# Kernel tuning notes

Measured on AMD Instinct MI355X. Metric: run time of the kernel, lower is better.

The kernel has to match this reference:

```python
import jax, jax.numpy as jnp
import numpy as np

EPS = 1e-5

def inorm(x, w, b):
    # InstanceNorm1d over token dim (axis=1), per (batch, feature); biased var
    m = x.mean(axis=1, keepdims=True)
    v = ((x - m) ** 2).mean(axis=1, keepdims=True)
    return (x - m) / jnp.sqrt(v + EPS) * w + b

def setup_inputs() -> dict:
    B, N, D, FH = 2, 512, 128, 512
    key = jax.random.key(0)
    ks = iter(jax.random.split(key, 48))
    rn = lambda shape, s=0.05: jax.random.normal(next(ks), shape, jnp.float32) * s
    inp = {
        'row_emb': jax.random.normal(next(ks), (B, N, D), jnp.float32),
        'col_emb': jax.random.normal(next(ks), (B, N, D), jnp.float32),
        'cost_mat': jax.random.uniform(next(ks), (B, N, N), jnp.float32),
        'coords': jax.random.uniform(next(ks), (B, N, 2), jnp.float32),
        'alpha': jnp.ones((1,), jnp.float32),
        # instance norm affine params (weight~1, bias~0)
        'n1_w': 1.0 + rn((D,)), 'n1_b': rn((D,)),
        'n2_w': 1.0 + rn((D,)), 'n2_b': rn((D,)),
        'n3_w': 1.0 + rn((D,)), 'n3_b': rn((D,)),
        'fn1_w': 1.0 + rn((D,)), 'fn1_b': rn((D,)),
        'fn2_w': 1.0 + rn((D,)), 'fn2_b': rn((D,)),
        # AFTFull projections (stored (in,out))
        'q_w': rn((D, D)), 'q_b': rn((D,)),
        'k_w': rn((D, D)), 'k_b': rn((D,)),
        'v_w': rn((D, D)), 'v_b': rn((D,)),
        'p_w': rn((D, D)), 'p_b': rn((D,)),
        'mhc_w': rn((D, D)), 'mhc_b': rn((D,)),
        # DistAngleFusion MLPs
        'dist_w1': rn((1, D)), 'dist_b1': rn((D,)),
        'dist_w2': rn((D, D)), 'dist_b2': rn((D,)),
        'ang_w1': rn((1, D)), 'ang_b1': rn((D,)),
        'ang_w2': rn((D, D)), 'ang_b2': rn((D,)),
        'gate_w': rn((2 * D, 1)), 'gate_b': rn((1,)),
        'outlin_w': rn((D, 1)), 'outlin_b': rn((1,)),
        # FeedForward
        'ffn_w1': rn((D, FH)), 'ffn_b1': rn((FH,)),
        'ffn_w2': rn((FH, D)), 'ffn_b2': rn((D,)),
    }
    return inp

def reference(row_emb, col_emb, cost_mat, coords, alpha,
              n1_w, n1_b, n2_w, n2_b, n3_w, n3_b, fn1_w, fn1_b, fn2_w, fn2_b,
              q_w, q_b, k_w, k_b, v_w, v_b, p_w, p_b, mhc_w, mhc_b,
              dist_w1, dist_b1, dist_w2, dist_b2,
              ang_w1, ang_b1, ang_w2, ang_b2,
              gate_w, gate_b, outlin_w, outlin_b,
              ffn_w1, ffn_b1, ffn_w2, ffn_b2):
    rn = inorm(row_emb, n1_w, n1_b)
    cn = inorm(col_emb, n2_w, n2_b)

    # DistAngleFusion: adapt_bias (B,N,N)
    diff = coords[:, :, None, :] - coords[:, None, :, :]  # (B,N,N,2)
    angles = jnp.arctan2(diff[..., 1], diff[..., 0])
    dist_e = jax.nn.relu(cost_mat[..., None] @ dist_w1 + dist_b1) @ dist_w2 + dist_b2  # (B,N,N,D)
    angle_e = jax.nn.relu(angles[..., None] @ ang_w1 + ang_b1) @ ang_w2 + ang_b2
    g = jax.nn.sigmoid(jnp.concatenate([dist_e, angle_e], axis=-1) @ gate_w + gate_b)  # (B,N,N,1)
    fused = g * dist_e + (1.0 - g) * angle_e
    adapt_bias = (fused @ outlin_w + outlin_b)[..., 0] * alpha  # (B,N,N)

    # AFTFull
    Q = jax.nn.sigmoid(rn @ q_w + q_b)          # (B,N,H)
    K = jax.nn.softmax(cn @ k_w + k_b, axis=1)  # softmax over tokens
    V = cn @ v_w + v_b
    eab = jnp.exp(jax.nn.softmax(adapt_bias, axis=-1))  # (B,N,N)
    eK = jnp.exp(K)
    num = jnp.einsum('bnm,bmh->bnh', eab, eK * V)
    den = jnp.einsum('bnm,bmh->bnh', eab, eK)
    Yt = (Q * (num / den)) @ p_w + p_b

    mh = inorm(Yt @ mhc_w + mhc_b, n3_w, n3_b)

    # TransformerFFN with instance norms
    x = inorm(rn + mh, fn1_w, fn1_b)
    ff = jax.nn.relu(x @ ffn_w1 + ffn_b1) @ ffn_w2 + ffn_b2
    return inorm(x + ff, fn2_w, fn2_b)
```

## Files before the change

### kernel.cpp

```cpp
#include <hip/hip_runtime.h>
#include <hip/hip_bf16.h>
#include <math.h>

#define Bn  2
#define Nn  512
#define Dn  128
#define FHn 512
#define BND (Bn*Nn*Dn)

typedef __hip_bfloat16 bf16;

__device__ __forceinline__ float cvt(float x) { return x; }
__device__ __forceinline__ float cvt(bf16 x) { return __bfloat162float(x); }
__device__ __forceinline__ float sigmoidf_(float x) { return 1.0f / (1.0f + expf(-x)); }
__device__ __forceinline__ bool is_bf16(const void* alpha) {
    return ((const unsigned short*)alpha)[0] == 0x3F80;
}

#define S_ 131072
#define WS_Q    (0 * S_)
#define WS_K    (1 * S_)
#define WS_V    (2 * S_)
#define WS_EK   (3 * S_)
#define WS_EKV  (4 * S_)
#define WS_EAB  (5 * S_)
#define WS_MH   (1 * S_)
#define WS_T    (2 * S_)
#define WS_OP   (3 * S_)
#define WS_ST   (9 * S_)

#define ST_IN_SC   0
#define ST_IN_SH   512
#define ST_X_SC    2048
#define ST_X_SH    2304
#define ST_PRE     3072
#define P_SC       1024
#define ST_TAB     4224

#define TAB_ANG 644
#define TAB_N   1288

#define SMEM_FLOATS 2568

struct KP {
    const void *row, *col, *cost, *coords, *alpha;
    const void *n1w, *n1b, *n2w, *n2b, *n3w, *n3b, *f1w, *f1b, *f2w, *f2b;
    const void *qw, *qb, *kw, *kb, *vw, *vb, *pw, *pb, *mw, *mb;
    const void *dw1, *db1, *dw2, *db2, *aw1, *ab1, *aw2, *ab2, *gw, *gb, *ow, *ob;
    const void *ffw1, *ffb1, *ffw2, *ffb2;
    void* out;
    float* ws;
};

__device__ __forceinline__ void blk_sum2(float& s, float& ss, volatile float* scr) {
#pragma unroll
    for (int off = 32; off > 0; off >>= 1) { s += __shfl_down(s, off); ss += __shfl_down(ss, off); }
    __syncthreads();
    int wave = threadIdx.x >> 6, lane = threadIdx.x & 63;
    if (lane == 0) { scr[wave] = s; scr[4 + wave] = ss; }
    __syncthreads();
    s = scr[0] + scr[1] + scr[2] + scr[3];
    ss = scr[4] + scr[5] + scr[6] + scr[7];
}

__device__ __forceinline__ float blk_sum1(float v, volatile float* scr) {
#pragma unroll
    for (int off = 32; off > 0; off >>= 1) v += __shfl_down(v, off);
    __syncthreads();
    int wave = threadIdx.x >> 6, lane = threadIdx.x & 63;
    if (lane == 0) scr[wave] = v;
    __syncthreads();
    return scr[0] + scr[1] + scr[2] + scr[3];
}

__device__ __forceinline__ float blk_max1(float v, volatile float* scr) {
#pragma unroll
    for (int off = 32; off > 0; off >>= 1) v = fmaxf(v, __shfl_down(v, off));
    __syncthreads();
    int wave = threadIdx.x >> 6, lane = threadIdx.x & 63;
    if (lane == 0) scr[wave] = v;
    __syncthreads();
    return fmaxf(fmaxf(scr[0], scr[1]), fmaxf(scr[2], scr[3]));
}

template <typename T>
__device__ void build_tables(const T* w1p, const T* b1p, const T* w2p,
                             const T* owp, const T* gwp, float* gtab, float* smem) {
    int tid = threadIdx.x;
    float* W  = smem;
    float* Bb = smem + 128;
    float* U  = smem + 256;
    float* Vv = smem + 384;
    float* Tt = smem + 512;
    int* RK   = (int*)(smem + 640);
    if (tid < 128) {
        float u = 0.f, v = 0.f;
#pragma unroll 4
        for (int d = 0; d < Dn; ++d) {
            float w2 = cvt(w2p[tid * Dn + d]);
            u += w2 * cvt(owp[d]);
            v += w2 * cvt(gwp[d]);
        }
        float w = cvt(w1p[tid]), b = cvt(b1p[tid]);
        U[tid] = u; Vv[tid] = v; W[tid] = w; Bb[tid] = b;
        Tt[tid] = (w != 0.f) ? (-b / w) : 3.0e38f;
    }
    __syncthreads();
    if (tid < 128) {
        float tk = Tt[tid]; int r = 0;
        for (int j = 0; j < 128; ++j) {
            float tj = Tt[j];
            r += (tj < tk) || (tj == tk && j < tid);
        }
        RK[tid] = r;
        gtab[r] = tk;
    }
    __syncthreads();
    if (tid <= 128) {
        int si = tid;
        float slS = 0, inS = 0, slT = 0, inT = 0;
        for (int k = 0; k < 128; ++k) {
            float w = W[k];
            if (w == 0.f) {
                float rb = fmaxf(Bb[k], 0.f);
                inS += rb * U[k];
                inT += rb * Vv[k];
            } else {
                bool act = (w > 0.f) ? (RK[k] < si) : (RK[k] >= si);
                if (act) {
                    slS += w * U[k];  inS += Bb[k] * U[k];
                    slT += w * Vv[k]; inT += Bb[k] * Vv[k];
                }
            }
        }
        gtab[128 + si] = slS;
        gtab[257 + si] = inS;
        gtab[386 + si] = slT;
        gtab[515 + si] = inT;
    }
}

__device__ __forceinline__ int bsearch128(const float* T, float c) {
    int lo = 0, hi = 128;
    while (lo < hi) { int mid = (lo + hi) >> 1; if (T[mid] <= c) lo = mid + 1; else hi = mid; }
    return lo;
}

template <typename T>
__device__ void phase0(const KP& p, float* st, float* smem) {
    float* scr = smem + 2560;
    int cid = blockIdx.x;
    int tid = threadIdx.x;
    {
        int which = cid >> 8, b = (cid >> 7) & 1, d = cid & 127;
        const T* src = (const T*)(which ? p.col : p.row) + (size_t)b * Nn * Dn + d;
        float x0 = cvt(src[(size_t)tid * Dn]);
        float x1 = cvt(src[(size_t)(tid + 256) * Dn]);
        float s = x0 + x1, ss = x0 * x0 + x1 * x1;
        blk_sum2(s, ss, scr);
        if (tid == 0) {
            float m = s * (1.f / Nn);
            float v = fmaxf(ss * (1.f / Nn) - m * m, 0.f);
            float rstd = rsqrtf(v + 1e-5f);
            const T* w = which ? (const T*)p.n2w : (const T*)p.n1w;
            const T* bb = which ? (const T*)p.n2b : (const T*)p.n1b;
            float sc = rstd * cvt(w[d]);
            st[ST_IN_SC + cid] = sc;
            st[ST_IN_SH + cid] = cvt(bb[d]) - m * sc;
        }
    }
    __syncthreads();
    if (cid == 128) {
        const T* db2 = (const T*)p.db2; const T* ab2 = (const T*)p.ab2;
        const T* ow = (const T*)p.ow;   const T* gw = (const T*)p.gw;
        float d2 = 0.f, a2 = 0.f, o = 0.f, g0 = 0.f, g1 = 0.f;
        if (tid < 128) {
            d2 = cvt(db2[tid]); a2 = cvt(ab2[tid]);
            o = cvt(ow[tid]); g0 = cvt(gw[tid]); g1 = cvt(gw[Dn + tid]);
        }
        float cds = d2 * o, cdt = d2 * g0, cas = a2 * o, cat = a2 * g1;
        blk_sum2(cds, cdt, scr);
        blk_sum2(cas, cat, scr);
        if (tid == 0) {
            float* pre = st + ST_PRE;
            pre[P_SC + 0] = cds; pre[P_SC + 1] = cdt;
            pre[P_SC + 2] = cas; pre[P_SC + 3] = cat;
            pre[P_SC + 4] = cvt(((const T*)p.gb)[0]);
            pre[P_SC + 5] = cvt(((const T*)p.ob)[0]);
            pre[P_SC + 6] = cvt(((const T*)p.alpha)[0]);
        }
    } else if (cid == 129) {
        build_tables<T>((const T*)p.dw1, (const T*)p.db1, (const T*)p.dw2,
                        (const T*)p.ow, (const T*)p.gw, st + ST_TAB, smem);
    } else if (cid == 130) {
        build_tables<T>((const T*)p.aw1, (const T*)p.ab1, (const T*)p.aw2,
                        (const T*)p.ow, (const T*)p.gw + Dn, st + ST_TAB + TAB_ANG, smem);
    }
}

template <typename T>
__device__ void phase1(const KP& p, float* st, float* smem) {
    int tid = threadIdx.x;
    int r0 = blockIdx.x * 2;
    int b = r0 >> 9;
    const T* row = (const T*)p.row; const T* col = (const T*)p.col;
    float* ws = p.ws;
    float* Q = ws + WS_Q; float* Kraw = ws + WS_K; float* V = ws + WS_V;

    float* lr = smem;
    float* lc = smem + 256;
    float* redq = smem + 512;
    float* redk = smem + 1024;
    float* redv = smem + 1536;
    {
        int r = tid >> 7, d = tid & 127;
        float scR = st[ST_IN_SC + b * 128 + d],       shR = st[ST_IN_SH + b * 128 + d];
        float scC = st[ST_IN_SC + 256 + b * 128 + d], shC = st[ST_IN_SH + 256 + b * 128 + d];
        lr[r * 128 + d] = cvt(row[(size_t)(r0 + r) * Dn + d]) * scR + shR;
        lc[r * 128 + d] = cvt(col[(size_t)(r0 + r) * Dn + d]) * scC + shC;
    }
    __syncthreads();
    {
        int h = tid & 127, half = tid >> 7;
        const T* qw = (const T*)p.qw; const T* kw = (const T*)p.kw; const T* vw = (const T*)p.vw;
        float q0 = 0, q1 = 0, ka = 0, kb_ = 0, v0 = 0, v1 = 0;
        int ks = half * 64;
#pragma unroll 8
        for (int k = ks; k < ks + 64; ++k) {
            float wq = cvt(qw[k * Dn + h]);
            float wk = cvt(kw[k * Dn + h]);
            float wv = cvt(vw[k * Dn + h]);
            q0 += lr[k] * wq;        q1 += lr[128 + k] * wq;
            ka += lc[k] * wk;        kb_ += lc[128 + k] * wk;
            v0 += lc[k] * wv;        v1 += lc[128 + k] * wv;
        }
        redq[half * 256 + h] = q0;  redq[half * 256 + 128 + h] = q1;
        redk[half * 256 + h] = ka;  redk[half * 256 + 128 + h] = kb_;
        redv[half * 256 + h] = v0;  redv[half * 256 + 128 + h] = v1;
    }
    __syncthreads();
    if (tid < 128) {
        int h = tid;
        float bq = cvt(((const T*)p.qb)[h]);
        float bk = cvt(((const T*)p.kb)[h]);
        float bv = cvt(((const T*)p.vb)[h]);
#pragma unroll
        for (int r = 0; r < 2; ++r) {
            Q[(r0 + r) * Dn + h]    = sigmoidf_(redq[r * 128 + h] + redq[256 + r * 128 + h] + bq);
            Kraw[(r0 + r) * Dn + h] = redk[r * 128 + h] + redk[256 + r * 128 + h] + bk;
            V[(r0 + r) * Dn + h]    = redv[r * 128 + h] + redv[256 + r * 128 + h] + bv;
        }
    }
    __syncthreads();

    float* abv = smem;
    float* red = smem + 512;
    float* tab = smem + 768;
    const float* gtab = st + ST_TAB;
    for (int e = tid; e < TAB_N; e += 256) tab[e] = gtab[e];
    __syncthreads();
    float* eab = ws + WS_EAB;
    const float* pre = st + ST_PRE;
    float cds = pre[P_SC + 0], cdt = pre[P_SC + 1], cas = pre[P_SC + 2], cat = pre[P_SC + 3];
    float gbias = pre[P_SC + 4], obias = pre[P_SC + 5], alpha = pre[P_SC + 6];
    const T* cost = (const T*)p.cost;
    const T* coords = (const T*)p.coords;

    for (int rr = 0; rr < 2; ++rr) {
        int rowi = r0 + rr;
        int bb_ = rowi >> 9, i = rowi & 511;
        float cix = cvt(coords[((size_t)bb_ * Nn + i) * 2 + 0]);
        float ciy = cvt(coords[((size_t)bb_ * Nn + i) * 2 + 1]);
        const T* crow = cost + (size_t)bb_ * Nn * Nn + (size_t)i * Nn;
#pragma unroll
        for (int jj = 0; jj < 2; ++jj) {
            int j = tid + jj * 256;
            float c = cvt(crow[j]);
            int si = bsearch128(tab, c);
            float sd = fmaf(tab[128 + si], c, tab[257 + si]) + cds;
            float td = fmaf(tab[386 + si], c, tab[515 + si]) + cdt;
            float dx = cix - cvt(coords[((size_t)bb_ * Nn + j) * 2 + 0]);
            float dy = ciy - cvt(coords[((size_t)bb_ * Nn + j) * 2 + 1]);
            float ang = (dx == 0.f && dy == 0.f) ? 0.f : atan2f(dy, dx);
            int ai = bsearch128(tab + TAB_ANG, ang);
            float sa = fmaf(tab[TAB_ANG + 128 + ai], ang, tab[TAB_ANG + 257 + ai]) + cas;
            float ta = fmaf(tab[TAB_ANG + 386 + ai], ang, tab[TAB_ANG + 515 + ai]) + cat;
            float gv = sigmoidf_(td + ta + gbias);
            abv[j] = alpha * (gv * sd + (1.f - gv) * sa + obias);
        }
        __syncthreads();
        float m = fmaxf(abv[tid], abv[tid + 256]);
        red[tid] = m; __syncthreads();
        for (int s = 128; s > 0; s >>= 1) {
            if (tid < s) red[tid] = fmaxf(red[tid], red[tid + s]);
            __syncthreads();
        }
        m = red[0];
        __syncthreads();
        float e0 = expf(abv[tid] - m), e1 = expf(abv[tid + 256] - m);
        red[tid] = e0 + e1; __syncthreads();
        for (int s = 128; s > 0; s >>= 1) {
            if (tid < s) red[tid] += red[tid + s];
            __syncthreads();
        }
        float rsum = 1.f / red[0];
        float* orow = eab + (size_t)rowi * Nn;
        orow[tid] = expf(e0 * rsum);
        orow[tid + 256] = expf(e1 * rsum);
        __syncthreads();
    }
}

__device__ void phase2(const KP& p, float* smem) {
    float* scr = smem + 2560;
    int tid = threadIdx.x;
    int c = blockIdx.x;
    int b = c >> 7, h = c & 127;
    float* ws = p.ws;
    const float* Kraw = ws + WS_K;
    const float* V = ws + WS_V;
    float* eK = ws + WS_EK;
    float* eKV = ws + WS_EKV;
    const float* kb = Kraw + (size_t)b * Nn * Dn + h;
    const float* vb = V + (size_t)b * Nn * Dn + h;
    float x0 = kb[(size_t)tid * Dn];
    float x1 = kb[(size_t)(tid + 256) * Dn];
    float mx = blk_max1(fmaxf(x0, x1), scr);
    float e0 = expf(x0 - mx), e1 = expf(x1 - mx);
    float s = blk_sum1(e0 + e1, scr);
    float rs = 1.f / s;
    size_t a0 = (size_t)b * Nn * Dn + (size_t)tid * Dn + h;
    size_t a1 = (size_t)b * Nn * Dn + (size_t)(tid + 256) * Dn + h;
    float ek0 = expf(e0 * rs), ek1 = expf(e1 * rs);
    eK[a0] = ek0;  eKV[a0] = ek0 * vb[(size_t)tid * Dn];
    eK[a1] = ek1;  eKV[a1] = ek1 * vb[(size_t)(tid + 256) * Dn];
}

template <typename T>
__device__ void phase3(const KP& p, float* smem) {
    int tid = threadIdx.x;
    int r0 = blockIdx.x * 2;
    int b = r0 >> 9;
    float* ws = p.ws;
    const float* eab = ws + WS_EAB;
    const float* eK = ws + WS_EK;
    const float* eKV = ws + WS_EKV;
    const float* Q = ws + WS_Q;
    float* mh = ws + WS_MH;

    float* ab   = smem;
    float* redn = smem + 1024;
    float* redd = smem + 1536;
    float* gl   = smem + 2048;
    float* yl   = smem + 2304;

    for (int e = tid; e < 1024; e += 256) {
        int r = e >> 9, j = e & 511;
        ab[e] = eab[(size_t)(r0 + r) * Nn + j];
    }
    __syncthreads();
    int h = tid & 127, half = tid >> 7;
    {
        float n0 = 0, n1 = 0, d0 = 0, d1 = 0;
        int j0 = half * 256;
        const float* ekb = eK + (size_t)b * Nn * Dn + h;
        const float* evb = eKV + (size_t)b * Nn * Dn + h;
#pragma unroll 4
        for (int j = j0; j < j0 + 256; ++j) {
            float ek = ekb[(size_t)j * Dn];
            float ev = evb[(size_t)j * Dn];
            n0 += ab[j] * ev;        d0 += ab[j] * ek;
            n1 += ab[512 + j] * ev;  d1 += ab[512 + j] * ek;
        }
        redn[half * 256 + h] = n0;  redn[half * 256 + 128 + h] = n1;
        redd[half * 256 + h] = d0;  redd[half * 256 + 128 + h] = d1;
    }
    __syncthreads();
    if (tid < 128) {
#pragma unroll
        for (int r = 0; r < 2; ++r) {
            float nu = redn[r * 128 + h] + redn[256 + r * 128 + h];
            float de = redd[r * 128 + h] + redd[256 + r * 128 + h];
            gl[r * 128 + h] = Q[(r0 + r) * Dn + h] * nu / de;
        }
    }
    __syncthreads();
    {
        const T* pw = (const T*)p.pw;
        float a0 = 0, a1 = 0;
        int ks = half * 64;
#pragma unroll 8
        for (int k = ks; k < ks + 64; ++k) {
            float w = cvt(pw[k * Dn + h]);
            a0 += gl[k] * w;
            a1 += gl[128 + k] * w;
        }
        redn[half * 256 + h] = a0;  redn[half * 256 + 128 + h] = a1;
    }
    __syncthreads();
    if (tid < 128) {
        float bp = cvt(((const T*)p.pb)[h]);
        yl[h] = redn[h] + redn[256 + h] + bp;
        yl[128 + h] = redn[128 + h] + redn[256 + 128 + h] + bp;
    }
    __syncthreads();
    {
        const T* mw = (const T*)p.mw;
        float a0 = 0, a1 = 0;
        int ks = half * 64;
#pragma unroll 8
        for (int k = ks; k < ks + 64; ++k) {
            float w = cvt(mw[k * Dn + h]);
            a0 += yl[k] * w;
            a1 += yl[128 + k] * w;
        }
        redn[half * 256 + h] = a0;  redn[half * 256 + 128 + h] = a1;
    }
    __syncthreads();
    if (tid < 128) {
        float bm = cvt(((const T*)p.mb)[h]);
        mh[(r0 + 0) * Dn + h] = redn[h] + redn[256 + h] + bm;
        mh[(r0 + 1) * Dn + h] = redn[128 + h] + redn[256 + 128 + h] + bm;
    }
}

template <typename T>
__device__ void phase45(const KP& p, float* st, float* smem) {
    float* scr = smem + 2560;
    int tid = threadIdx.x;
    int c = blockIdx.x;
    int b = c >> 7, d = c & 127;
    const float* mh = p.ws + WS_MH;
    const float* mp = mh + (size_t)b * Nn * Dn + d;
    float m0 = mp[(size_t)tid * Dn], m1 = mp[(size_t)(tid + 256) * Dn];
    float s = m0 + m1, ss = m0 * m0 + m1 * m1;
    blk_sum2(s, ss, scr);
    float mm = s * (1.f / Nn);
    float vv = fmaxf(ss * (1.f / Nn) - mm * mm, 0.f);
    float rstd = rsqrtf(vv + 1e-5f);
    float scM = rstd * cvt(((const T*)p.n3w)[d]);
    float shM = cvt(((const T*)p.n3b)[d]) - mm * scM;
    const T* row = (const T*)p.row;
    float scI = st[ST_IN_SC + c], shI = st[ST_IN_SH + c];
    const T* rp = row + (size_t)b * Nn * Dn + d;
    float* tp = p.ws + WS_T + (size_t)b * Nn * Dn + d;
    float x0 = cvt(rp[(size_t)tid * Dn]) * scI + shI + m0 * scM + shM;
    float x1 = cvt(rp[(size_t)(tid + 256) * Dn]) * scI + shI + m1 * scM + shM;
    tp[(size_t)tid * Dn] = x0;
    tp[(size_t)(tid + 256) * Dn] = x1;
    __syncthreads();
    float s2 = x0 + x1, ss2 = x0 * x0 + x1 * x1;
    blk_sum2(s2, ss2, scr);
    if (tid == 0) {
        float m = s2 * (1.f / Nn);
        float v = fmaxf(ss2 * (1.f / Nn) - m * m, 0.f);
        float r = rsqrtf(v + 1e-5f);
        float sc = r * cvt(((const T*)p.f1w)[d]);
        st[ST_X_SC + c] = sc;
        st[ST_X_SH + c] = cvt(((const T*)p.f1b)[d]) - m * sc;
    }
}

template <typename T>
__device__ void phase6(const KP& p, float* st, float* smem) {
    int tid = threadIdx.x;
    int r0 = blockIdx.x * 2;
    int b = r0 >> 9;
    const float* t = p.ws + WS_T;
    float* outpre = p.ws + WS_OP;
    const T* w1 = (const T*)p.ffw1; const T* b1 = (const T*)p.ffb1;
    const T* w2 = (const T*)p.ffw2; const T* b2 = (const T*)p.ffb2;

    float* xl = smem;
    float* hl = smem + 256;
    float* red = smem + 1280;
    {
        int r = tid >> 7, d = tid & 127;
        int c = b * 128 + d;
        xl[r * 128 + d] = t[(r0 + r) * Dn + d] * st[ST_X_SC + c] + st[ST_X_SH + c];
    }
    __syncthreads();
    {
        int f0 = tid, f1 = tid + 256;
        float a00 = 0, a10 = 0, a01 = 0, a11 = 0;
#pragma unroll 4
        for (int k = 0; k < Dn; ++k) {
            float w0 = cvt(w1[k * FHn + f0]);
            float wA = cvt(w1[k * FHn + f1]);
            a00 += xl[k] * w0;       a10 += xl[128 + k] * w0;
            a01 += xl[k] * wA;       a11 += xl[128 + k] * wA;
        }
        float bb0 = cvt(b1[f0]), bbA = cvt(b1[f1]);
        hl[f0] = fmaxf(a00 + bb0, 0.f);        hl[512 + f0] = fmaxf(a10 + bb0, 0.f);
        hl[f1] = fmaxf(a01 + bbA, 0.f);        hl[512 + f1] = fmaxf(a11 + bbA, 0.f);
    }
    __syncthreads();
    {
        int d = tid & 127, half = tid >> 7;
        int k0 = half * 256;
        float c0 = 0, c1 = 0;
#pragma unroll 8
        for (int k = k0; k < k0 + 256; ++k) {
            float w = cvt(w2[k * Dn + d]);
            c0 += hl[k] * w;
            c1 += hl[512 + k] * w;
        }
        red[half * 256 + d] = c0;  red[half * 256 + 128 + d] = c1;
    }
    __syncthreads();
    if (tid < 128) {
        float bb2 = cvt(b2[tid]);
        outpre[(r0 + 0) * Dn + tid] = xl[tid] + red[tid] + red[256 + tid] + bb2;
        outpre[(r0 + 1) * Dn + tid] = xl[128 + tid] + red[128 + tid] + red[256 + 128 + tid] + bb2;
    }
}

template <typename T>
__device__ void phase78(const KP& p, float* smem) {
    float* scr = smem + 2560;
    int tid = threadIdx.x;
    int c = blockIdx.x;
    int b = c >> 7, d = c & 127;
    const float* op = p.ws + WS_OP;
    const float* sp = op + (size_t)b * Nn * Dn + d;
    float x0 = sp[(size_t)tid * Dn], x1 = sp[(size_t)(tid + 256) * Dn];
    float s = x0 + x1, ss = x0 * x0 + x1 * x1;
    blk_sum2(s, ss, scr);
    float m = s * (1.f / Nn);
    float v = fmaxf(ss * (1.f / Nn) - m * m, 0.f);
    float rstd = rsqrtf(v + 1e-5f);
    float sc = rstd * cvt(((const T*)p.f2w)[d]);
    float sh = cvt(((const T*)p.f2b)[d]) - m * sc;
    T* out = (T*)p.out + (size_t)b * Nn * Dn + d;
    out[(size_t)tid * Dn] = (T)(x0 * sc + sh);
    out[(size_t)(tid + 256) * Dn] = (T)(x1 * sc + sh);
}

#define PH_WRAP(name, call_bf, call_f)                                        \
__global__ __launch_bounds__(256) void name(KP p) {                           \
    __shared__ float smem[SMEM_FLOATS];                                       \
    float* st = p.ws + WS_ST; (void)st;                                       \
    if (is_bf16(p.alpha)) { call_bf; } else { call_f; }                       \
}

PH_WRAP(k_head,  phase0<bf16>(p, st, smem),  phase0<float>(p, st, smem))
PH_WRAP(k_qkveab, phase1<bf16>(p, st, smem), phase1<float>(p, st, smem))
__global__ __launch_bounds__(256) void k_kekv(KP p) {
    __shared__ float smem[SMEM_FLOATS];
    phase2(p, smem);
}
PH_WRAP(k_attn,  phase3<bf16>(p, smem),      phase3<float>(p, smem))
PH_WRAP(k_mid,   phase45<bf16>(p, st, smem), phase45<float>(p, st, smem))
PH_WRAP(k_ffn,   phase6<bf16>(p, st, smem),  phase6<float>(p, st, smem))
PH_WRAP(k_tail,  phase78<bf16>(p, smem),     phase78<float>(p, smem))

extern "C" void kernel_launch(void* const* d_in, const int* in_sizes, int n_in,
                              void* d_out, int out_size, void* d_ws, size_t ws_size,
                              hipStream_t stream) {
    KP p;
    p.row = d_in[0];  p.col = d_in[1];  p.cost = d_in[2];  p.coords = d_in[3];
    p.alpha = d_in[4];
    p.n1w = d_in[5];  p.n1b = d_in[6];  p.n2w = d_in[7];  p.n2b = d_in[8];
    p.n3w = d_in[9];  p.n3b = d_in[10]; p.f1w = d_in[11]; p.f1b = d_in[12];
    p.f2w = d_in[13]; p.f2b = d_in[14];
    p.qw = d_in[15];  p.qb = d_in[16];  p.kw = d_in[17];  p.kb = d_in[18];
    p.vw = d_in[19];  p.vb = d_in[20];  p.pw = d_in[21];  p.pb = d_in[22];
    p.mw = d_in[23];  p.mb = d_in[24];
    p.dw1 = d_in[25]; p.db1 = d_in[26]; p.dw2 = d_in[27]; p.db2 = d_in[28];
    p.aw1 = d_in[29]; p.ab1 = d_in[30]; p.aw2 = d_in[31]; p.ab2 = d_in[32];
    p.gw = d_in[33];  p.gb = d_in[34];  p.ow = d_in[35];  p.ob = d_in[36];
    p.ffw1 = d_in[37]; p.ffb1 = d_in[38]; p.ffw2 = d_in[39]; p.ffb2 = d_in[40];
    p.out = d_out;
    p.ws = (float*)d_ws;

    k_head<<<512, 256, 0, stream>>>(p);
    k_qkveab<<<512, 256, 0, stream>>>(p);
    k_kekv<<<256, 256, 0, stream>>>(p);
    k_attn<<<512, 256, 0, stream>>>(p);
    k_mid<<<256, 256, 0, stream>>>(p);
    k_ffn<<<512, 256, 0, stream>>>(p);
    k_tail<<<256, 256, 0, stream>>>(p);
}
```

Measured before the change: 260.6 us.

## Process four rows per block in attention and FFN kernels with 512 threads

The attention-aggregation kernel and the FFN kernel now handle four token rows per block instead of two. Blocks grow to 512 threads and the grid is halved. Each load of eK/eKV and of the projection and FFN weights is reused across four rows, roughly halving redundant global/L2 traffic for those operands. In exchange there are fewer blocks (256) to spread across CUs, larger shared-memory footprints, and more accumulator registers per thread.

```diff
diff --git a/kernel.cpp b/kernel.cpp
--- a/kernel.cpp
+++ b/kernel.cpp
@@ -339,7 +339,7 @@
 template <typename T>
 __device__ void phase3(const KP& p, float* smem) {
     int tid = threadIdx.x;
-    int r0 = blockIdx.x * 2;
+    int r0 = blockIdx.x * 4;
     int b = r0 >> 9;
     float* ws = p.ws;
     const float* eab = ws + WS_EAB;
@@ -349,78 +349,93 @@
     float* mh = ws + WS_MH;
 
     float* ab   = smem;
-    float* redn = smem + 1024;
-    float* redd = smem + 1536;
-    float* gl   = smem + 2048;
-    float* yl   = smem + 2304;
-
-    for (int e = tid; e < 1024; e += 256) {
-        int r = e >> 9, j = e & 511;
-        ab[e] = eab[(size_t)(r0 + r) * Nn + j];
-    }
-    __syncthreads();
-    int h = tid & 127, half = tid >> 7;
-    {
-        float n0 = 0, n1 = 0, d0 = 0, d1 = 0;
-        int j0 = half * 256;
+    float* redn = smem + 2048;
+    float* redd = smem + 4096;
+    float* gl   = smem + 6144;
+    float* yl   = smem + 6656;
+
+    {
+        float4* ab4 = (float4*)ab;
+        const float4* g4 = (const float4*)(eab + (size_t)r0 * Nn);
+        ab4[tid] = g4[tid];
+    }
+    __syncthreads();
+    int h = tid & 127, q = tid >> 7;
+    {
+        float num[4] = {0,0,0,0}, den[4] = {0,0,0,0};
+        int j0 = q * 128;
         const float* ekb = eK + (size_t)b * Nn * Dn + h;
         const float* evb = eKV + (size_t)b * Nn * Dn + h;
 #pragma unroll 4
-        for (int j = j0; j < j0 + 256; ++j) {
+        for (int j = j0; j < j0 + 128; ++j) {
             float ek = ekb[(size_t)j * Dn];
             float ev = evb[(size_t)j * Dn];
-            n0 += ab[j] * ev;        d0 += ab[j] * ek;
-            n1 += ab[512 + j] * ev;  d1 += ab[512 + j] * ek;
-        }
-        redn[half * 256 + h] = n0;  redn[half * 256 + 128 + h] = n1;
-        redd[half * 256 + h] = d0;  redd[half * 256 + 128 + h] = d1;
+#pragma unroll
+            for (int r = 0; r < 4; ++r) {
+                num[r] += ab[r * 512 + j] * ev;
+                den[r] += ab[r * 512 + j] * ek;
+            }
+        }
+#pragma unroll
+        for (int r = 0; r < 4; ++r) {
+            redn[q * 512 + r * 128 + h] = num[r];
+            redd[q * 512 + r * 128 + h] = den[r];
+        }
     }
     __syncthreads();
     if (tid < 128) {
 #pragma unroll
-        for (int r = 0; r < 2; ++r) {
-            float nu = redn[r * 128 + h] + redn[256 + r * 128 + h];
-            float de = redd[r * 128 + h] + redd[256 + r * 128 + h];
+        for (int r = 0; r < 4; ++r) {
+            float nu = redn[r * 128 + h] + redn[512 + r * 128 + h]
+                     + redn[1024 + r * 128 + h] + redn[1536 + r * 128 + h];
+            float de = redd[r * 128 + h] + redd[512 + r * 128 + h]
+                     + redd[1024 + r * 128 + h] + redd[1536 + r * 128 + h];
             gl[r * 128 + h] = Q[(r0 + r) * Dn + h] * nu / de;
         }
     }
     __syncthreads();
     {
         const T* pw = (const T*)p.pw;
-        float a0 = 0, a1 = 0;
-        int ks = half * 64;
+        float acc[4] = {0,0,0,0};
+        int ks = q * 32;
 #pragma unroll 8
-        for (int k = ks; k < ks + 64; ++k) {
+        for (int k = ks; k < ks + 32; ++k) {
             float w = cvt(pw[k * Dn + h]);
-            a0 += gl[k] * w;
-            a1 += gl[128 + k] * w;
-        }
-        redn[half * 256 + h] = a0;  redn[half * 256 + 128 + h] = a1;
+#pragma unroll
+            for (int r = 0; r < 4; ++r) acc[r] += gl[r * 128 + k] * w;
+        }
+#pragma unroll
+        for (int r = 0; r < 4; ++r) redn[q * 512 + r * 128 + h] = acc[r];
     }
     __syncthreads();
     if (tid < 128) {
         float bp = cvt(((const T*)p.pb)[h]);
-        yl[h] = redn[h] + redn[256 + h] + bp;
-        yl[128 + h] = redn[128 + h] + redn[256 + 128 + h] + bp;
+#pragma unroll
+        for (int r = 0; r < 4; ++r)
+            yl[r * 128 + h] = redn[r * 128 + h] + redn[512 + r * 128 + h]
+                            + redn[1024 + r * 128 + h] + redn[1536 + r * 128 + h] + bp;
     }
     __syncthreads();
     {
         const T* mw = (const T*)p.mw;
-        float a0 = 0, a1 = 0;
-        int ks = half * 64;
+        float acc[4] = {0,0,0,0};
+        int ks = q * 32;
 #pragma unroll 8
-        for (int k = ks; k < ks + 64; ++k) {
+        for (int k = ks; k < ks + 32; ++k) {
             float w = cvt(mw[k * Dn + h]);
-            a0 += yl[k] * w;
-            a1 += yl[128 + k] * w;
-        }
-        redn[half * 256 + h] = a0;  redn[half * 256 + 128 + h] = a1;
+#pragma unroll
+            for (int r = 0; r < 4; ++r) acc[r] += yl[r * 128 + k] * w;
+        }
+#pragma unroll
+        for (int r = 0; r < 4; ++r) redn[q * 512 + r * 128 + h] = acc[r];
     }
     __syncthreads();
     if (tid < 128) {
         float bm = cvt(((const T*)p.mb)[h]);
-        mh[(r0 + 0) * Dn + h] = redn[h] + redn[256 + h] + bm;
-        mh[(r0 + 1) * Dn + h] = redn[128 + h] + redn[256 + 128 + h] + bm;
+#pragma unroll
+        for (int r = 0; r < 4; ++r)
+            mh[(r0 + r) * Dn + h] = redn[r * 128 + h] + redn[512 + r * 128 + h]
+                                  + redn[1024 + r * 128 + h] + redn[1536 + r * 128 + h] + bm;
     }
 }
 
@@ -464,7 +479,7 @@
 template <typename T>
 __device__ void phase6(const KP& p, float* st, float* smem) {
     int tid = threadIdx.x;
-    int r0 = blockIdx.x * 2;
+    int r0 = blockIdx.x * 4;
     int b = r0 >> 9;
     const float* t = p.ws + WS_T;
     float* outpre = p.ws + WS_OP;
@@ -472,8 +487,8 @@
     const T* w2 = (const T*)p.ffw2; const T* b2 = (const T*)p.ffb2;
 
     float* xl = smem;
-    float* hl = smem + 256;
-    float* red = smem + 1280;
+    float* hl = smem + 512;
+    float* red = smem + 2560;
     {
         int r = tid >> 7, d = tid & 127;
         int c = b * 128 + d;
@@ -481,37 +496,41 @@
     }
     __syncthreads();
     {
-        int f0 = tid, f1 = tid + 256;
-        float a00 = 0, a10 = 0, a01 = 0, a11 = 0;
+        int f = tid;
+        float a[4] = {0,0,0,0};
 #pragma unroll 4
         for (int k = 0; k < Dn; ++k) {
-            float w0 = cvt(w1[k * FHn + f0]);
-            float wA = cvt(w1[k * FHn + f1]);
-            a00 += xl[k] * w0;       a10 += xl[128 + k] * w0;
-            a01 += xl[k] * wA;       a11 += xl[128 + k] * wA;
-        }
-        float bb0 = cvt(b1[f0]), bbA = cvt(b1[f1]);
-        hl[f0] = fmaxf(a00 + bb0, 0.f);        hl[512 + f0] = fmaxf(a10 + bb0, 0.f);
-        hl[f1] = fmaxf(a01 + bbA, 0.f);        hl[512 + f1] = fmaxf(a11 + bbA, 0.f);
-    }
-    __syncthreads();
-    {
-        int d = tid & 127, half = tid >> 7;
-        int k0 = half * 256;
-        float c0 = 0, c1 = 0;
+            float w = cvt(w1[k * FHn + f]);
+#pragma unroll
+            for (int r = 0; r < 4; ++r) a[r] += xl[r * 128 + k] * w;
+        }
+        float bb1 = cvt(b1[f]);
+#pragma unroll
+        for (int r = 0; r < 4; ++r) hl[r * 512 + f] = fmaxf(a[r] + bb1, 0.f);
+    }
+    __syncthreads();
+    {
+        int d = tid & 127, q = tid >> 7;
+        int k0 = q * 128;
+        float a[4] = {0,0,0,0};
 #pragma unroll 8
-        for (int k = k0; k < k0 + 256; ++k) {
+        for (int k = k0; k < k0 + 128; ++k) {
             float w = cvt(w2[k * Dn + d]);
-            c0 += hl[k] * w;
-            c1 += hl[512 + k] * w;
-        }
-        red[half * 256 + d] = c0;  red[half * 256 + 128 + d] = c1;
+#pragma unroll
+            for (int r = 0; r < 4; ++r) a[r] += hl[r * 512 + k] * w;
+        }
+#pragma unroll
+        for (int r = 0; r < 4; ++r) red[q * 512 + r * 128 + d] = a[r];
     }
     __syncthreads();
     if (tid < 128) {
         float bb2 = cvt(b2[tid]);
-        outpre[(r0 + 0) * Dn + tid] = xl[tid] + red[tid] + red[256 + tid] + bb2;
-        outpre[(r0 + 1) * Dn + tid] = xl[128 + tid] + red[128 + tid] + red[256 + 128 + tid] + bb2;
+#pragma unroll
+        for (int r = 0; r < 4; ++r) {
+            float sum = red[r * 128 + tid] + red[512 + r * 128 + tid]
+                      + red[1024 + r * 128 + tid] + red[1536 + r * 128 + tid];
+            outpre[(r0 + r) * Dn + tid] = xl[r * 128 + tid] + sum + bb2;
+        }
     }
 }
 
@@ -549,9 +568,18 @@
     __shared__ float smem[SMEM_FLOATS];
     phase2(p, smem);
 }
-PH_WRAP(k_attn,  phase3<bf16>(p, smem),      phase3<float>(p, smem))
+__global__ __launch_bounds__(512) void k_attn(KP p) {
+    __shared__ float smem[7168];
+    if (is_bf16(p.alpha)) phase3<bf16>(p, smem);
+    else                  phase3<float>(p, smem);
+}
 PH_WRAP(k_mid,   phase45<bf16>(p, st, smem), phase45<float>(p, st, smem))
-PH_WRAP(k_ffn,   phase6<bf16>(p, st, smem),  phase6<float>(p, st, smem))
+__global__ __launch_bounds__(512) void k_ffn(KP p) {
+    __shared__ float smem[4608];
+    float* st = p.ws + WS_ST;
+    if (is_bf16(p.alpha)) phase6<bf16>(p, st, smem);
+    else                  phase6<float>(p, st, smem);
+}
 PH_WRAP(k_tail,  phase78<bf16>(p, smem),     phase78<float>(p, smem))
 
 extern "C" void kernel_launch(void* const* d_in, const int* in_sizes, int n_in,
@@ -576,8 +604,8 @@
     k_head<<<512, 256, 0, stream>>>(p);
     k_qkveab<<<512, 256, 0, stream>>>(p);
     k_kekv<<<256, 256, 0, stream>>>(p);
-    k_attn<<<512, 256, 0, stream>>>(p);
+    k_attn<<<256, 512, 0, stream>>>(p);
     k_mid<<<256, 256, 0, stream>>>(p);
-    k_ffn<<<512, 256, 0, stream>>>(p);
+    k_ffn<<<256, 512, 0, stream>>>(p);
     k_tail<<<256, 256, 0, stream>>>(p);
 }
```

Measured after the change: 242.4 us. 7.0% less time.
